# Kernel tuning notes

Hardware: AMD Instinct MI355X
Metric: run time of the kernel (lower is better)

## Reference

```python
import jax, jax.numpy as jnp
import numpy as np

B, N, H, F = 256, 32, 256, 7
T = N * (N - 1) // 2  # 496
LIM_LO, LIM_HI = 0.499, 0.501  # torch ContinuousBernoulli stability lims
EPS = 1.1920929e-07  # float32 eps, torch clamp_probs


def _gru_cell(x, h, Wih, Whh, bih, bhh):
    # torch.nn.GRUCell math, gate order (r, z, n)
    gi = x @ Wih.T + bih
    gh = h @ Whh.T + bhh
    i_r, i_z, i_n = jnp.split(gi, 3, axis=-1)
    h_r, h_z, h_n = jnp.split(gh, 3, axis=-1)
    r = jax.nn.sigmoid(i_r + h_r)
    zg = jax.nn.sigmoid(i_z + h_z)
    n = jnp.tanh(i_n + r * h_n)
    return (1.0 - zg) * n + zg * h


def setup_inputs() -> dict:
    key = jax.random.key(0)
    ks = jax.random.split(key, 16)
    s = 1.0 / np.sqrt(H)  # torch GRUCell/Linear init scale
    # one-hot node features (NDist.sample_node_features hardcodes 7 classes)
    idx = jax.random.randint(ks[1], (B, N), 0, F)
    node_features = jax.nn.one_hot(idx, F, dtype=jnp.float32)
    return {
        "z": jax.random.normal(ks[0], (B, H), dtype=jnp.float32),
        "node_features": node_features,
        "u": jax.random.uniform(ks[2], (B, T), dtype=jnp.float32),
        "Wih_node": jax.random.uniform(ks[3], (3 * H, 2 * F + H), minval=-s, maxval=s),
        "Whh_node": jax.random.uniform(ks[4], (3 * H, H), minval=-s, maxval=s),
        "bih_node": jax.random.uniform(ks[5], (3 * H,), minval=-s, maxval=s),
        "bhh_node": jax.random.uniform(ks[6], (3 * H,), minval=-s, maxval=s),
        "Wih_graph": jax.random.uniform(ks[7], (3 * H, H), minval=-s, maxval=s),
        "Whh_graph": jax.random.uniform(ks[8], (3 * H, H), minval=-s, maxval=s),
        "bih_graph": jax.random.uniform(ks[9], (3 * H,), minval=-s, maxval=s),
        "bhh_graph": jax.random.uniform(ks[10], (3 * H,), minval=-s, maxval=s),
        "Ws1": jax.random.uniform(ks[11], (64, H), minval=-s, maxval=s),
        "bs1": jax.random.uniform(ks[12], (64,), minval=-s, maxval=s),
        "Ws2": jax.random.uniform(ks[13], (1, 64), minval=-1.0 / 8, maxval=1.0 / 8),
        "bs2": jax.random.uniform(ks[14], (1,), minval=-1.0 / 8, maxval=1.0 / 8),
    }


def _edge_params(z, node_features, Wih_node, Whh_node, bih_node, bhh_node,
                 Wih_graph, Whh_graph, bih_graph, bhh_graph, Ws1, bs1, Ws2, bs2):
    nf_seq = jnp.swapaxes(node_features, 0, 1)  # [N, B, F]

    def outer_step(graph_h, i):
        nf_i = jnp.take(node_features, i, axis=1)  # [B, F]

        def inner_step(node_h, xs):
            j, nf_j = xs
            edge_in = jnp.concatenate([nf_i, nf_j, node_h], axis=-1)
            new_h = _gru_cell(edge_in, node_h, Wih_node, Whh_node, bih_node, bhh_node)
            node_h = jnp.where(j > i, new_h, node_h)  # only steps j in (i, N) update state
            hid = jax.nn.relu(node_h @ Ws1.T + bs1)
            prob = jax.nn.sigmoid(hid @ Ws2.T + bs2)[:, 0]  # [B]
            return node_h, prob

        node_h, probs = jax.lax.scan(inner_step, graph_h, (jnp.arange(N), nf_seq))
        graph_h = _gru_cell(node_h, graph_h, Wih_graph, Whh_graph, bih_graph, bhh_graph)
        return graph_h, probs  # probs [N, B]

    _, grid = jax.lax.scan(outer_step, z, jnp.arange(N - 1))  # [N-1, N, B]
    grid = jnp.transpose(grid, (2, 0, 1))  # [B, N-1, N]
    ti, tj = np.triu_indices(N, 1)  # row-major order = original i-loop hstack order
    return grid[:, ti, tj]  # [B, T]


def _cb_rsample(probs, u):
    # torch ContinuousBernoulli icdf with clamp_probs and unstable-region passthrough
    p = jnp.clip(probs, EPS, 1.0 - EPS)
    outside = (p < LIM_LO) | (p > LIM_HI)
    cut = jnp.where(outside, p, LIM_LO)
    stable = (jnp.log1p(-cut + u * (2.0 * cut - 1.0)) - jnp.log1p(-cut)) / (
        jnp.log(cut) - jnp.log1p(-cut))
    return jnp.where(outside, stable, u)


def reference(z, node_features, u, Wih_node, Whh_node, bih_node, bhh_node,
              Wih_graph, Whh_graph, bih_graph, bhh_graph, Ws1, bs1, Ws2, bs2):
    params = _edge_params(z, node_features, Wih_node, Whh_node, bih_node, bhh_node,
                          Wih_graph, Whh_graph, bih_graph, bhh_graph, Ws1, bs1, Ws2, bs2)
    edges = _cb_rsample(params, u)  # [B, T]
    # Original get_triu_idx enumerates anti-ordered diagonals: offset N-1 down to 1.
    r_d = np.concatenate([np.arange(d) for d in range(1, N)])
    c_d = np.concatenate([np.arange(d) + (N - d) for d in range(1, N)])
    adj = jnp.zeros((B, N, N), dtype=edges.dtype)
    adj = adj.at[:, r_d, c_d].set(edges).at[:, c_d, r_d].set(edges)
    x = node_features.reshape(B * N, F)
    batch = jnp.repeat(jnp.arange(B, dtype=jnp.int32), N)
    return x, adj, batch
```

## Files before the change

kernel.cpp:

```cpp
#include <hip/hip_runtime.h>
#include <hip/hip_fp16.h>
#include <math.h>

#define BB 256
#define NN 32
#define HH 256
#define FF 7
#define TT 496

typedef _Float16 f16x2 __attribute__((ext_vector_type(2)));
typedef _Float16 f16x4 __attribute__((ext_vector_type(4)));
typedef _Float16 f16x8 __attribute__((ext_vector_type(8)));

#if defined(__has_builtin)
#  if __has_builtin(__builtin_amdgcn_fdot2)
#    define HAS_FDOT2 1
#  endif
#endif

__device__ __forceinline__ float dot2f(f16x2 a, f16x2 b, float c) {
#ifdef HAS_FDOT2
  return __builtin_amdgcn_fdot2(a, b, c, false);
#else
  return fmaf((float)a[1], (float)b[1], fmaf((float)a[0], (float)b[0], c));
#endif
}

#define SH2(V, L) __builtin_shufflevector(V, V, 2 * (L), 2 * (L) + 1)
#define SH01(V) __builtin_shufflevector(V, V, 0, 1)
#define SH23(V) __builtin_shufflevector(V, V, 2, 3)

#define H_WREG 0
#define H_WLDS 98304
#define H_WSTR 131072
#define H_WTG  262144
#define H_AB   655360
#define H_GB   666112
#define H_WS1  667648
#define F_HB    342016
#define F_PROBS 342272

#define S_WREG_END 98304
#define S_WLDS_END 131072
#define S_WSTR_END 262144
#define S_WTG_END  655360
#define S_AB_END   666112
#define S_GB_END   667648
#define S_WS1_END  684032
#define PREP_N     684288

__device__ __forceinline__ float weff(const float* Wih, const float* Whh, int k, int o) {
  if (o < 512) return Wih[o * 270 + 14 + k] + Whh[o * 256 + k];
  if (o < 768) return Wih[o * 270 + 14 + k];
  return Whh[(o - 256) * 256 + k];
}

__global__ void prep_kernel(const float* __restrict__ Wih_node,
                            const float* __restrict__ Whh_node,
                            const float* __restrict__ bih_node,
                            const float* __restrict__ bhh_node,
                            const float* __restrict__ Wih_graph,
                            const float* __restrict__ Whh_graph,
                            const float* __restrict__ bih_graph,
                            const float* __restrict__ bhh_graph,
                            const float* __restrict__ Ws1,
                            float* __restrict__ ws) {
  int idx = blockIdx.x * blockDim.x + threadIdx.x;
  if (idx >= PREP_N) return;
  __half* hw = (__half*)ws;
  if (idx < S_WREG_END) {
    int e = idx & 7, s = idx >> 3;
    int oc = s & 255, r = s >> 8;
    int pr = r % 12, kp = r / 12;
    int q = e >> 1, kb = e & 1;
    int k = kp * 64 + pr * 2 + kb;
    int o = oc + (q << 8);
    hw[H_WREG + idx] = __float2half(weff(Wih_node, Whh_node, k, o));
  } else if (idx < S_WLDS_END) {
    int i = idx - S_WREG_END;
    int e = i & 7, s = i >> 3;
    int oc = s & 255, r = s >> 8;
    int pr = r % 4, kp = r / 4;
    int q = e >> 1, kb = e & 1;
    int k = kp * 64 + 24 + pr * 2 + kb;
    int o = oc + (q << 8);
    hw[H_WLDS + i] = __float2half(weff(Wih_node, Whh_node, k, o));
  } else if (idx < S_WSTR_END) {
    int i = idx - S_WLDS_END;
    int e = i & 7, s = i >> 3;
    int oc = s & 255, r = s >> 8;
    int pr = r % 16, kp = r / 16;
    int q = e >> 1, kb = e & 1;
    int k = kp * 64 + 32 + pr * 2 + kb;
    int o = oc + (q << 8);
    hw[H_WSTR + i] = __float2half(weff(Wih_node, Whh_node, k, o));
  } else if (idx < S_WTG_END) {
    int i = idx - S_WSTR_END;
    int e = i & 3, s = i >> 2;
    int kb = e & 1, ob = e >> 1;
    int oc2 = s % 768, kpair = s / 768;
    int k = 2 * kpair + kb, o = 2 * oc2 + ob;
    float v = (o < 768) ? Wih_graph[o * 256 + k] : Whh_graph[(o - 768) * 256 + k];
    hw[H_WTG + i] = __float2half(v);
  } else if (idx < S_AB_END) {
    int i = idx - S_WTG_END;
    float v;
    if (i < 5376) {
      int ci = i / 768, o = i % 768;
      v = Wih_node[o * 270 + ci] + bih_node[o] + ((o < 512) ? bhh_node[o] : 0.f);
    } else {
      int i2 = i - 5376;
      int cj = i2 / 768, o = i2 % 768;
      v = Wih_node[o * 270 + 7 + cj];
    }
    hw[H_AB + i] = __float2half(v);
  } else if (idx < S_GB_END) {
    int i = idx - S_AB_END;
    float v = (i < 768) ? bih_graph[i] : bhh_graph[i - 768];
    hw[H_GB + i] = __float2half(v);
  } else if (idx < S_WS1_END) {
    int i = idx - S_GB_END;
    int kk = i & 15, r = i >> 4;
    int u2 = r & 63, kq = r >> 6;
    hw[H_WS1 + i] = __float2half(Ws1[u2 * 256 + kq * 16 + kk]);
  } else {
    int u = idx - S_WS1_END;
    ws[F_HB + u] = bhh_node[512 + u];
  }
}

#define PAIR(Wv, Hv, L) { \
  f16x2 h2_ = SH2(Hv, L); \
  s0 = dot2f(h2_, SH2(Wv, 0), s0); \
  s1 = dot2f(h2_, SH2(Wv, 1), s1); \
  s2 = dot2f(h2_, SH2(Wv, 2), s2); \
  s3 = dot2f(h2_, SH2(Wv, 3), s3); }

#define MLPPART() { \
  const int u2_ = t & 63, kq_ = t >> 6; \
  const f16x8* w1p_ = (const f16x8*)s_ws1 + ((kq_ << 6) + u2_) * 2; \
  f16x8 wa_ = w1p_[0], wb_ = w1p_[1]; \
  const f16x8* nhp_ = (const f16x8*)nh2 + (kq_ << 1); \
  f16x8 ha_ = nhp_[0], hb_ = nhp_[1]; \
  float p_ = 0.f; \
  p_ = dot2f(SH2(ha_, 0), SH2(wa_, 0), p_); \
  p_ = dot2f(SH2(ha_, 1), SH2(wa_, 1), p_); \
  p_ = dot2f(SH2(ha_, 2), SH2(wa_, 2), p_); \
  p_ = dot2f(SH2(ha_, 3), SH2(wa_, 3), p_); \
  p_ = dot2f(SH2(hb_, 0), SH2(wb_, 0), p_); \
  p_ = dot2f(SH2(hb_, 1), SH2(wb_, 1), p_); \
  p_ = dot2f(SH2(hb_, 2), SH2(wb_, 2), p_); \
  p_ = dot2f(SH2(hb_, 3), SH2(wb_, 3), p_); \
  part2[kq_][u2_] = p_; }

#define MLPRED(dst) { \
  int v_ = t - 960; \
  float hv_ = part2[0][v_]+part2[1][v_]+part2[2][v_]+part2[3][v_] \
            + part2[4][v_]+part2[5][v_]+part2[6][v_]+part2[7][v_] \
            + part2[8][v_]+part2[9][v_]+part2[10][v_]+part2[11][v_] \
            + part2[12][v_]+part2[13][v_]+part2[14][v_]+part2[15][v_] + s_bs1[v_]; \
  hv_ = fmaxf(hv_, 0.f); \
  float c2_ = hv_ * s_ws2[v_]; \
  for (int off_ = 32; off_ > 0; off_ >>= 1) c2_ += __shfl_down(c2_, off_); \
  if (v_ == 0) dst = 1.f / (1.f + expf(-(c2_ + s_bs2))); }

__global__ __launch_bounds__(1024) void rnn_kernel(
    const float* __restrict__ z,
    const float* __restrict__ nf,
    const float* __restrict__ bs1,
    const float* __restrict__ Ws2,
    const float* __restrict__ bs2,
    float* __restrict__ ws) {
  __shared__ __align__(16) __half s_wl[32768];
  __shared__ __align__(16) __half s_a2[5376];
  __shared__ __align__(16) __half s_b2[5376];
  __shared__ __align__(16) __half s_ws1[16384];
  __shared__ __align__(16) __half s_gbi[768];
  __shared__ __align__(16) __half s_gbh[768];
  __shared__ __align__(16) float s_hb[256];
  __shared__ __align__(16) float nh[256];
  __shared__ __align__(16) __half nh2[256];
  __shared__ __align__(16) float gh2[256];
  __shared__ __align__(16) __half gh2h[256];
  __shared__ __align__(16) float part[4][1024];
  __shared__ __align__(16) float part2[16][64];
  __shared__ float s_bs1[64], s_ws2[64];
  __shared__ int cls[NN];
  __shared__ float s_bs2;

  const int b = blockIdx.x, t = threadIdx.x;
  const __half* hws = (const __half*)ws;
  float* probs = ws + F_PROBS + (size_t)b * TT;

  {
    f16x8* dst = (f16x8*)s_wl;
    const f16x8* src = (const f16x8*)(hws + H_WLDS);
    for (int x = t; x < 4096; x += 1024) dst[x] = src[x];
  }
  for (int x = t; x < 5376; x += 1024) {
    s_a2[x] = hws[H_AB + x];
    s_b2[x] = hws[H_AB + 5376 + x];
  }
  for (int x = t; x < 16384; x += 1024) s_ws1[x] = hws[H_WS1 + x];
  if (t < 768) {
    s_gbi[t] = hws[H_GB + t];
    s_gbh[t] = hws[H_GB + 768 + t];
  }
  if (t < 256) {
    s_hb[t] = ws[F_HB + t];
    float v = z[b * 256 + t];
    nh[t] = v; gh2[t] = v;
    __half vh = __float2half(v);
    nh2[t] = vh; gh2h[t] = vh;
  }
  if (t < 64) { s_bs1[t] = bs1[t]; s_ws2[t] = Ws2[t]; }
  if (t == 0) s_bs2 = bs2[0];
  if (t < NN) {
    const float* row = nf + (b * NN + t) * FF;
    int c = 0;
#pragma unroll
    for (int q = 1; q < FF; ++q)
      if (row[q] > 0.5f) c = q;
    cls[t] = c;
  }

  const int kp = t >> 8;
  const int oc = t & 255;

  const f16x8* wreg = (const f16x8*)(hws + H_WREG) + (kp * 12) * 256 + oc;
  f16x8 W0 = wreg[0 * 256],  W1 = wreg[1 * 256],  W2 = wreg[2 * 256];
  f16x8 W3 = wreg[3 * 256],  W4 = wreg[4 * 256],  W5 = wreg[5 * 256];
  f16x8 W6 = wreg[6 * 256],  W7 = wreg[7 * 256],  W8 = wreg[8 * 256];
  f16x8 W9 = wreg[9 * 256],  W10 = wreg[10 * 256], W11 = wreg[11 * 256];

  const f16x8* stp = (const f16x8*)(hws + H_WSTR) + (kp * 16) * 256 + oc;
  const f16x8* swl = (const f16x8*)s_wl + (kp * 4) * 256 + oc;
  const f16x8* hv8 = (const f16x8*)nh2 + (kp << 3);
  __syncthreads();

  int base = 0;
  for (int i = 0; i < NN - 1; ++i) {
    const __half* ArH = s_a2 + cls[i] * 768;

    for (int j = i + 1; j < NN; ++j) {
      const __half* BrH = s_b2 + cls[j] * 768;
      const bool pend = (j > i + 1);
      asm volatile("" : "+v"(W0), "+v"(W1), "+v"(W2), "+v"(W3), "+v"(W4),
                        "+v"(W5), "+v"(W6), "+v"(W7), "+v"(W8), "+v"(W9),
                        "+v"(W10), "+v"(W11));
      float s0 = 0.f, s1 = 0.f, s2 = 0.f, s3 = 0.f;
      f16x8 S0 = stp[0 * 256], S1 = stp[1 * 256], S2 = stp[2 * 256], S3 = stp[3 * 256];
      f16x8 S4 = stp[4 * 256], S5 = stp[5 * 256], S6 = stp[6 * 256], S7 = stp[7 * 256];
      f16x8 H0 = hv8[0], H1 = hv8[1], H2 = hv8[2];
      PAIR(W0, H0, 0) PAIR(W1, H0, 1) PAIR(W2, H0, 2) PAIR(W3, H0, 3)
      PAIR(W4, H1, 0) PAIR(W5, H1, 1) PAIR(W6, H1, 2) PAIR(W7, H1, 3)
      PAIR(W8, H2, 0) PAIR(W9, H2, 1) PAIR(W10, H2, 2) PAIR(W11, H2, 3)
      f16x8 S8 = stp[8 * 256], S9 = stp[9 * 256], S10 = stp[10 * 256], S11 = stp[11 * 256];
      f16x8 S12 = stp[12 * 256], S13 = stp[13 * 256], S14 = stp[14 * 256], S15 = stp[15 * 256];
      {
        f16x8 H3 = hv8[3];
        f16x8 L0 = swl[0 * 256], L1 = swl[1 * 256], L2 = swl[2 * 256], L3 = swl[3 * 256];
        PAIR(L0, H3, 0) PAIR(L1, H3, 1) PAIR(L2, H3, 2) PAIR(L3, H3, 3)
      }
      {
        f16x8 H4 = hv8[4], H5 = hv8[5], H6 = hv8[6], H7 = hv8[7];
        PAIR(S0, H4, 0) PAIR(S1, H4, 1) PAIR(S2, H4, 2) PAIR(S3, H4, 3)
        PAIR(S4, H5, 0) PAIR(S5, H5, 1) PAIR(S6, H5, 2) PAIR(S7, H5, 3)
        PAIR(S8, H6, 0) PAIR(S9, H6, 1) PAIR(S10, H6, 2) PAIR(S11, H6, 3)
        PAIR(S12, H7, 0) PAIR(S13, H7, 1) PAIR(S14, H7, 2) PAIR(S15, H7, 3)
      }
      part[kp][oc] = s0;
      part[kp][oc + 256] = s1;
      part[kp][oc + 512] = s2;
      part[kp][oc + 768] = s3;
      if (pend) MLPPART()
      __syncthreads();
      if (t < 256) {
        const int u = t;
        float pr  = part[0][u]       + part[1][u]       + part[2][u]       + part[3][u];
        float pz  = part[0][256 + u] + part[1][256 + u] + part[2][256 + u] + part[3][256 + u];
        float pin = part[0][512 + u] + part[1][512 + u] + part[2][512 + u] + part[3][512 + u];
        float phn = part[0][768 + u] + part[1][768 + u] + part[2][768 + u] + part[3][768 + u];
        float ar = (float)ArH[u]       + (float)BrH[u];
        float az = (float)ArH[256 + u] + (float)BrH[256 + u];
        float an = (float)ArH[512 + u] + (float)BrH[512 + u];
        float r  = 1.f / (1.f + expf(-(pr + ar)));
        float zg = 1.f / (1.f + expf(-(pz + az)));
        float n2 = tanhf(pin + an + r * (phn + s_hb[u]));
        float nv = (1.f - zg) * n2 + zg * nh[u];
        nh[u] = nv;
        nh2[u] = __float2half(nv);
      } else if (pend && t >= 960) {
        MLPRED(probs[base + j - i - 2])
      }
      __syncthreads();
    }

    {
      if (t < 768) {
        const __half* hsrc2 = (t < 384) ? nh2 : gh2h;
        const f16x8* hg = (const f16x8*)hsrc2;
        const f16x4* wg = (const f16x4*)(hws + H_WTG) + t;
        float g0 = 0.f, g1 = 0.f;
#pragma unroll 8
        for (int c = 0; c < 32; ++c) {
          f16x8 Hc = hg[c];
          f16x4 a0 = wg[(c * 4 + 0) * 768];
          f16x4 a1 = wg[(c * 4 + 1) * 768];
          f16x4 a2 = wg[(c * 4 + 2) * 768];
          f16x4 a3 = wg[(c * 4 + 3) * 768];
          g0 = dot2f(SH2(Hc, 0), SH01(a0), g0); g1 = dot2f(SH2(Hc, 0), SH23(a0), g1);
          g0 = dot2f(SH2(Hc, 1), SH01(a1), g0); g1 = dot2f(SH2(Hc, 1), SH23(a1), g1);
          g0 = dot2f(SH2(Hc, 2), SH01(a2), g0); g1 = dot2f(SH2(Hc, 2), SH23(a2), g1);
          g0 = dot2f(SH2(Hc, 3), SH01(a3), g0); g1 = dot2f(SH2(Hc, 3), SH23(a3), g1);
        }
        ((float*)part)[(t << 1)] = g0;
        ((float*)part)[(t << 1) + 1] = g1;
      }
      MLPPART()
      __syncthreads();
      if (t < 256) {
        const int u = t;
        const float* pf = (const float*)part;
        float gir = pf[u]        + (float)s_gbi[u];
        float giz = pf[256 + u]  + (float)s_gbi[256 + u];
        float gin = pf[512 + u]  + (float)s_gbi[512 + u];
        float ghr = pf[768 + u]  + (float)s_gbh[u];
        float ghz = pf[1024 + u] + (float)s_gbh[256 + u];
        float ghn = pf[1280 + u] + (float)s_gbh[512 + u];
        float r  = 1.f / (1.f + expf(-(gir + ghr)));
        float zg = 1.f / (1.f + expf(-(giz + ghz)));
        float n2 = tanhf(gin + r * ghn);
        float nv = (1.f - zg) * n2 + zg * gh2[u];
        gh2[u] = nv; nh[u] = nv;
        __half vh = __float2half(nv);
        gh2h[u] = vh; nh2[u] = vh;
      } else if (t >= 960) {
        MLPRED(probs[base + NN - 2 - i])
      }
      __syncthreads();
    }
    base += NN - 1 - i;
  }
}

__global__ void edges_kernel(const float* __restrict__ u,
                             const float* __restrict__ ws,
                             float* __restrict__ adj) {
  int idx = blockIdx.x * blockDim.x + threadIdx.x;
  if (idx >= BB * TT) return;
  int b = idx / TT, t = idx % TT;
  float prob = ws[F_PROBS + (size_t)b * TT + t];
  float uu = u[idx];
  const float EPSF = 1.1920929e-07f;
  float p = fminf(fmaxf(prob, EPSF), 1.0f - EPSF);
  bool outside = (p < 0.499f) || (p > 0.501f);
  float cut = outside ? p : 0.499f;
  float stable = (log1pf(fmaf(uu, 2.f * cut - 1.f, -cut)) - log1pf(-cut)) /
                 (logf(cut) - log1pf(-cut));
  float e = outside ? stable : uu;
  int d = (int)((1.0f + sqrtf(1.0f + 8.0f * (float)t)) * 0.5f);
  while (d * (d + 1) / 2 <= t) ++d;
  while (d * (d - 1) / 2 > t) --d;
  int k = t - d * (d - 1) / 2;
  int r = k, c = k + (NN - d);
  adj[((size_t)b * NN + r) * NN + c] = e;
  adj[((size_t)b * NN + c) * NN + r] = e;
}

__global__ void xb_kernel(const float* __restrict__ nf,
                          float* __restrict__ out_x,
                          float* __restrict__ out_batch) {
  int idx = blockIdx.x * blockDim.x + threadIdx.x;
  if (idx < BB * NN * FF) out_x[idx] = nf[idx];
  if (idx < BB * NN) out_batch[idx] = (float)(idx >> 5);
}

extern "C" void kernel_launch(void* const* d_in, const int* in_sizes, int n_in,
                              void* d_out, int out_size, void* d_ws, size_t ws_size,
                              hipStream_t stream) {
  const float* z         = (const float*)d_in[0];
  const float* nf        = (const float*)d_in[1];
  const float* u         = (const float*)d_in[2];
  const float* Wih_node  = (const float*)d_in[3];
  const float* Whh_node  = (const float*)d_in[4];
  const float* bih_node  = (const float*)d_in[5];
  const float* bhh_node  = (const float*)d_in[6];
  const float* Wih_graph = (const float*)d_in[7];
  const float* Whh_graph = (const float*)d_in[8];
  const float* bih_graph = (const float*)d_in[9];
  const float* bhh_graph = (const float*)d_in[10];
  const float* Ws1       = (const float*)d_in[11];
  const float* bs1       = (const float*)d_in[12];
  const float* Ws2       = (const float*)d_in[13];
  const float* bs2       = (const float*)d_in[14];

  float* ws = (float*)d_ws;
  float* out_x   = (float*)d_out;
  float* out_adj = out_x + BB * NN * FF;
  float* out_batch = out_x + BB * NN * FF + (size_t)BB * NN * NN;

  hipMemsetAsync(out_adj, 0, (size_t)BB * NN * NN * sizeof(float), stream);
  prep_kernel<<<(PREP_N + 255) / 256, 256, 0, stream>>>(
      Wih_node, Whh_node, bih_node, bhh_node,
      Wih_graph, Whh_graph, bih_graph, bhh_graph, Ws1, ws);
  rnn_kernel<<<BB, 1024, 0, stream>>>(z, nf, bs1, Ws2, bs2, ws);
  xb_kernel<<<(BB * NN * FF + 255) / 256, 256, 0, stream>>>(nf, out_x, out_batch);
  edges_kernel<<<(BB * TT + 255) / 256, 256, 0, stream>>>(u, ws, out_adj);
}
```

Baseline: 2.707 ms.

## Keep more node-GRU weights in registers, use fast exp/rcp activations, split Ws1 LDS

Each thread now holds 20 instead of 12 f16x8 weight vectors of the node GRU in registers, and half as many are streamed from global memory each step. The per-step streamed global load is cut from 16 to 8 vectors, and the loads are interleaved with the dot products. Sigmoid and tanh switch to hardware exp2 and rcp intrinsics instead of expf and tanhf. The MLP Ws1 weights are split into two LDS arrays so each thread does one 16-byte read per array. The extra registers risk spilling at 1024 threads per block, and the fast intrinsics lose a little accuracy.

```diff
diff --git a/kernel.cpp b/kernel.cpp
--- a/kernel.cpp
+++ b/kernel.cpp
@@ -26,27 +26,38 @@
 #endif
 }
 
+__device__ __forceinline__ float fsigm(float x) {
+  float e = __builtin_amdgcn_exp2f(x * -1.44269504f);
+  return __builtin_amdgcn_rcpf(1.f + e);
+}
+__device__ __forceinline__ float ftanh(float x) {
+  float e = __builtin_amdgcn_exp2f(x * 2.88539008f);
+  return 1.f - 2.f * __builtin_amdgcn_rcpf(e + 1.f);
+}
+
 #define SH2(V, L) __builtin_shufflevector(V, V, 2 * (L), 2 * (L) + 1)
 #define SH01(V) __builtin_shufflevector(V, V, 0, 1)
 #define SH23(V) __builtin_shufflevector(V, V, 2, 3)
 
 #define H_WREG 0
-#define H_WLDS 98304
-#define H_WSTR 131072
+#define H_WLDS 163840
+#define H_WSTR 196608
 #define H_WTG  262144
 #define H_AB   655360
 #define H_GB   666112
-#define H_WS1  667648
+#define H_WS1A 667648
+#define H_WS1B 675840
 #define F_HB    342016
 #define F_PROBS 342272
 
-#define S_WREG_END 98304
-#define S_WLDS_END 131072
+#define S_WREG_END 163840
+#define S_WLDS_END 196608
 #define S_WSTR_END 262144
 #define S_WTG_END  655360
 #define S_AB_END   666112
 #define S_GB_END   667648
-#define S_WS1_END  684032
+#define S_WS1A_END 675840
+#define S_WS1B_END 684032
 #define PREP_N     684288
 
 __device__ __forceinline__ float weff(const float* Wih, const float* Whh, int k, int o) {
@@ -71,7 +82,7 @@
   if (idx < S_WREG_END) {
     int e = idx & 7, s = idx >> 3;
     int oc = s & 255, r = s >> 8;
-    int pr = r % 12, kp = r / 12;
+    int pr = r % 20, kp = r / 20;
     int q = e >> 1, kb = e & 1;
     int k = kp * 64 + pr * 2 + kb;
     int o = oc + (q << 8);
@@ -82,16 +93,16 @@
     int oc = s & 255, r = s >> 8;
     int pr = r % 4, kp = r / 4;
     int q = e >> 1, kb = e & 1;
-    int k = kp * 64 + 24 + pr * 2 + kb;
+    int k = kp * 64 + 40 + pr * 2 + kb;
     int o = oc + (q << 8);
     hw[H_WLDS + i] = __float2half(weff(Wih_node, Whh_node, k, o));
   } else if (idx < S_WSTR_END) {
     int i = idx - S_WLDS_END;
     int e = i & 7, s = i >> 3;
     int oc = s & 255, r = s >> 8;
-    int pr = r % 16, kp = r / 16;
+    int pr = r % 8, kp = r / 8;
     int q = e >> 1, kb = e & 1;
-    int k = kp * 64 + 32 + pr * 2 + kb;
+    int k = kp * 64 + 48 + pr * 2 + kb;
     int o = oc + (q << 8);
     hw[H_WSTR + i] = __float2half(weff(Wih_node, Whh_node, k, o));
   } else if (idx < S_WTG_END) {
@@ -118,13 +129,18 @@
     int i = idx - S_AB_END;
     float v = (i < 768) ? bih_graph[i] : bhh_graph[i - 768];
     hw[H_GB + i] = __float2half(v);
-  } else if (idx < S_WS1_END) {
+  } else if (idx < S_WS1A_END) {
     int i = idx - S_GB_END;
-    int kk = i & 15, r = i >> 4;
+    int kk = i & 7, r = i >> 3;
     int u2 = r & 63, kq = r >> 6;
-    hw[H_WS1 + i] = __float2half(Ws1[u2 * 256 + kq * 16 + kk]);
+    hw[H_WS1A + i] = __float2half(Ws1[u2 * 256 + kq * 16 + kk]);
+  } else if (idx < S_WS1B_END) {
+    int i = idx - S_WS1A_END;
+    int kk = i & 7, r = i >> 3;
+    int u2 = r & 63, kq = r >> 6;
+    hw[H_WS1B + i] = __float2half(Ws1[u2 * 256 + kq * 16 + 8 + kk]);
   } else {
-    int u = idx - S_WS1_END;
+    int u = idx - S_WS1B_END;
     ws[F_HB + u] = bhh_node[512 + u];
   }
 }
@@ -138,8 +154,8 @@
 
 #define MLPPART() { \
   const int u2_ = t & 63, kq_ = t >> 6; \
-  const f16x8* w1p_ = (const f16x8*)s_ws1 + ((kq_ << 6) + u2_) * 2; \
-  f16x8 wa_ = w1p_[0], wb_ = w1p_[1]; \
+  f16x8 wa_ = ((const f16x8*)s_ws1a)[(kq_ << 6) + u2_]; \
+  f16x8 wb_ = ((const f16x8*)s_ws1b)[(kq_ << 6) + u2_]; \
   const f16x8* nhp_ = (const f16x8*)nh2 + (kq_ << 1); \
   f16x8 ha_ = nhp_[0], hb_ = nhp_[1]; \
   float p_ = 0.f; \
@@ -162,7 +178,7 @@
   hv_ = fmaxf(hv_, 0.f); \
   float c2_ = hv_ * s_ws2[v_]; \
   for (int off_ = 32; off_ > 0; off_ >>= 1) c2_ += __shfl_down(c2_, off_); \
-  if (v_ == 0) dst = 1.f / (1.f + expf(-(c2_ + s_bs2))); }
+  if (v_ == 0) dst = fsigm(c2_ + s_bs2); }
 
 __global__ __launch_bounds__(1024) void rnn_kernel(
     const float* __restrict__ z,
@@ -174,7 +190,8 @@
   __shared__ __align__(16) __half s_wl[32768];
   __shared__ __align__(16) __half s_a2[5376];
   __shared__ __align__(16) __half s_b2[5376];
-  __shared__ __align__(16) __half s_ws1[16384];
+  __shared__ __align__(16) __half s_ws1a[8192];
+  __shared__ __align__(16) __half s_ws1b[8192];
   __shared__ __align__(16) __half s_gbi[768];
   __shared__ __align__(16) __half s_gbh[768];
   __shared__ __align__(16) float s_hb[256];
@@ -201,7 +218,10 @@
     s_a2[x] = hws[H_AB + x];
     s_b2[x] = hws[H_AB + 5376 + x];
   }
-  for (int x = t; x < 16384; x += 1024) s_ws1[x] = hws[H_WS1 + x];
+  for (int x = t; x < 8192; x += 1024) {
+    s_ws1a[x] = hws[H_WS1A + x];
+    s_ws1b[x] = hws[H_WS1B + x];
+  }
   if (t < 768) {
     s_gbi[t] = hws[H_GB + t];
     s_gbh[t] = hws[H_GB + 768 + t];
@@ -227,13 +247,14 @@
   const int kp = t >> 8;
   const int oc = t & 255;
 
-  const f16x8* wreg = (const f16x8*)(hws + H_WREG) + (kp * 12) * 256 + oc;
-  f16x8 W0 = wreg[0 * 256],  W1 = wreg[1 * 256],  W2 = wreg[2 * 256];
-  f16x8 W3 = wreg[3 * 256],  W4 = wreg[4 * 256],  W5 = wreg[5 * 256];
-  f16x8 W6 = wreg[6 * 256],  W7 = wreg[7 * 256],  W8 = wreg[8 * 256];
-  f16x8 W9 = wreg[9 * 256],  W10 = wreg[10 * 256], W11 = wreg[11 * 256];
-
-  const f16x8* stp = (const f16x8*)(hws + H_WSTR) + (kp * 16) * 256 + oc;
+  const f16x8* wreg = (const f16x8*)(hws + H_WREG) + (kp * 20) * 256 + oc;
+  f16x8 W0 = wreg[0 * 256],  W1 = wreg[1 * 256],  W2 = wreg[2 * 256],  W3 = wreg[3 * 256];
+  f16x8 W4 = wreg[4 * 256],  W5 = wreg[5 * 256],  W6 = wreg[6 * 256],  W7 = wreg[7 * 256];
+  f16x8 W8 = wreg[8 * 256],  W9 = wreg[9 * 256],  W10 = wreg[10 * 256], W11 = wreg[11 * 256];
+  f16x8 W12 = wreg[12 * 256], W13 = wreg[13 * 256], W14 = wreg[14 * 256], W15 = wreg[15 * 256];
+  f16x8 W16 = wreg[16 * 256], W17 = wreg[17 * 256], W18 = wreg[18 * 256], W19 = wreg[19 * 256];
+
+  const f16x8* stp = (const f16x8*)(hws + H_WSTR) + (kp * 8) * 256 + oc;
   const f16x8* swl = (const f16x8*)s_wl + (kp * 4) * 256 + oc;
   const f16x8* hv8 = (const f16x8*)nh2 + (kp << 3);
   __syncthreads();
@@ -247,27 +268,31 @@
       const bool pend = (j > i + 1);
       asm volatile("" : "+v"(W0), "+v"(W1), "+v"(W2), "+v"(W3), "+v"(W4),
                         "+v"(W5), "+v"(W6), "+v"(W7), "+v"(W8), "+v"(W9),
-                        "+v"(W10), "+v"(W11));
+                        "+v"(W10), "+v"(W11), "+v"(W12), "+v"(W13), "+v"(W14),
+                        "+v"(W15), "+v"(W16), "+v"(W17), "+v"(W18), "+v"(W19));
       float s0 = 0.f, s1 = 0.f, s2 = 0.f, s3 = 0.f;
       f16x8 S0 = stp[0 * 256], S1 = stp[1 * 256], S2 = stp[2 * 256], S3 = stp[3 * 256];
+      {
+        f16x8 H0 = hv8[0], H1 = hv8[1];
+        PAIR(W0, H0, 0) PAIR(W1, H0, 1) PAIR(W2, H0, 2) PAIR(W3, H0, 3)
+        PAIR(W4, H1, 0) PAIR(W5, H1, 1) PAIR(W6, H1, 2) PAIR(W7, H1, 3)
+      }
       f16x8 S4 = stp[4 * 256], S5 = stp[5 * 256], S6 = stp[6 * 256], S7 = stp[7 * 256];
-      f16x8 H0 = hv8[0], H1 = hv8[1], H2 = hv8[2];
-      PAIR(W0, H0, 0) PAIR(W1, H0, 1) PAIR(W2, H0, 2) PAIR(W3, H0, 3)
-      PAIR(W4, H1, 0) PAIR(W5, H1, 1) PAIR(W6, H1, 2) PAIR(W7, H1, 3)
-      PAIR(W8, H2, 0) PAIR(W9, H2, 1) PAIR(W10, H2, 2) PAIR(W11, H2, 3)
-      f16x8 S8 = stp[8 * 256], S9 = stp[9 * 256], S10 = stp[10 * 256], S11 = stp[11 * 256];
-      f16x8 S12 = stp[12 * 256], S13 = stp[13 * 256], S14 = stp[14 * 256], S15 = stp[15 * 256];
       {
-        f16x8 H3 = hv8[3];
+        f16x8 H2 = hv8[2], H3 = hv8[3], H4 = hv8[4];
+        PAIR(W8, H2, 0)  PAIR(W9, H2, 1)  PAIR(W10, H2, 2) PAIR(W11, H2, 3)
+        PAIR(W12, H3, 0) PAIR(W13, H3, 1) PAIR(W14, H3, 2) PAIR(W15, H3, 3)
+        PAIR(W16, H4, 0) PAIR(W17, H4, 1) PAIR(W18, H4, 2) PAIR(W19, H4, 3)
+      }
+      {
+        f16x8 H5 = hv8[5];
         f16x8 L0 = swl[0 * 256], L1 = swl[1 * 256], L2 = swl[2 * 256], L3 = swl[3 * 256];
-        PAIR(L0, H3, 0) PAIR(L1, H3, 1) PAIR(L2, H3, 2) PAIR(L3, H3, 3)
+        PAIR(L0, H5, 0) PAIR(L1, H5, 1) PAIR(L2, H5, 2) PAIR(L3, H5, 3)
       }
       {
-        f16x8 H4 = hv8[4], H5 = hv8[5], H6 = hv8[6], H7 = hv8[7];
-        PAIR(S0, H4, 0) PAIR(S1, H4, 1) PAIR(S2, H4, 2) PAIR(S3, H4, 3)
-        PAIR(S4, H5, 0) PAIR(S5, H5, 1) PAIR(S6, H5, 2) PAIR(S7, H5, 3)
-        PAIR(S8, H6, 0) PAIR(S9, H6, 1) PAIR(S10, H6, 2) PAIR(S11, H6, 3)
-        PAIR(S12, H7, 0) PAIR(S13, H7, 1) PAIR(S14, H7, 2) PAIR(S15, H7, 3)
+        f16x8 H6 = hv8[6], H7 = hv8[7];
+        PAIR(S0, H6, 0) PAIR(S1, H6, 1) PAIR(S2, H6, 2) PAIR(S3, H6, 3)
+        PAIR(S4, H7, 0) PAIR(S5, H7, 1) PAIR(S6, H7, 2) PAIR(S7, H7, 3)
       }
       part[kp][oc] = s0;
       part[kp][oc + 256] = s1;
@@ -284,9 +309,9 @@
         float ar = (float)ArH[u]       + (float)BrH[u];
         float az = (float)ArH[256 + u] + (float)BrH[256 + u];
         float an = (float)ArH[512 + u] + (float)BrH[512 + u];
-        float r  = 1.f / (1.f + expf(-(pr + ar)));
-        float zg = 1.f / (1.f + expf(-(pz + az)));
-        float n2 = tanhf(pin + an + r * (phn + s_hb[u]));
+        float r  = fsigm(pr + ar);
+        float zg = fsigm(pz + az);
+        float n2 = ftanh(pin + an + r * (phn + s_hb[u]));
         float nv = (1.f - zg) * n2 + zg * nh[u];
         nh[u] = nv;
         nh2[u] = __float2half(nv);
@@ -328,9 +353,9 @@
         float ghr = pf[768 + u]  + (float)s_gbh[u];
         float ghz = pf[1024 + u] + (float)s_gbh[256 + u];
         float ghn = pf[1280 + u] + (float)s_gbh[512 + u];
-        float r  = 1.f / (1.f + expf(-(gir + ghr)));
-        float zg = 1.f / (1.f + expf(-(giz + ghz)));
-        float n2 = tanhf(gin + r * ghn);
+        float r  = fsigm(gir + ghr);
+        float zg = fsigm(giz + ghz);
+        float n2 = ftanh(gin + r * ghn);
         float nv = (1.f - zg) * n2 + zg * gh2[u];
         gh2[u] = nv; nh[u] = nv;
         __half vh = __float2half(nv);
```

New measurement: 2.791 ms. 1.03x slower.
